# Optimization experiments

Measured on AMD Instinct MI355X. Metric: run time of the kernel, lower is better.

The kernel has to match this reference:

```python
import jax, jax.numpy as jnp
import numpy as np

B, N, C = 4, 2048, 256
H = 8
DH = C // H
WIN = 16
SCALE = DH ** -0.5


def setup_inputs() -> dict:
    key = jax.random.key(0)
    k1, k2, k3, k4 = jax.random.split(key, 4)
    x = jax.random.normal(k1, (B, N, C), dtype=jnp.float32)
    # qkv: nn.Linear(dim, 3*dim, bias=False); store as [C, 3C] for x @ W
    W_qkv = jax.random.normal(k2, (C, 3 * C), dtype=jnp.float32) * (C ** -0.5)
    # proj: nn.Linear(dim, dim) with bias
    W_proj = jax.random.normal(k3, (C, C), dtype=jnp.float32) * (C ** -0.5)
    b_proj = jax.random.normal(k4, (C,), dtype=jnp.float32) * 0.01
    return {"x": x, "W_qkv": W_qkv, "W_proj": W_proj, "b_proj": b_proj}


def reference(x, W_qkv, W_proj, b_proj):
    Bs, Ns, Cs = x.shape
    # qkv projection -> q, k, v each [B, H, N, Dh]
    qkv = (x @ W_qkv).reshape(Bs, Ns, 3, H, DH).transpose(2, 0, 3, 1, 4)
    q, k, v = qkv[0], qkv[1], qkv[2]

    # --- global dense attention ---
    attn_global = jax.nn.softmax(jnp.einsum('bhnd,bhmd->bhnm', q, k) * SCALE, axis=-1)
    x_global = jnp.einsum('bhnm,bhmd->bhnd', attn_global, v)  # [B,H,N,Dh]

    # --- non-overlapping local window attention (vectorized over windows) ---
    nw = Ns // WIN
    qw = q.reshape(Bs, H, nw, WIN, DH)
    kw = k.reshape(Bs, H, nw, WIN, DH)
    vw = v.reshape(Bs, H, nw, WIN, DH)
    attn_local = jax.nn.softmax(jnp.einsum('bhwid,bhwjd->bhwij', qw, kw) * SCALE, axis=-1)
    x_local = jnp.einsum('bhwij,bhwjd->bhwid', attn_local, vw).reshape(Bs, H, Ns, DH)

    # combine, merge heads, output projection
    x_out = (x_global + x_local).transpose(0, 2, 1, 3).reshape(Bs, Ns, Cs)
    x_out = x_out @ W_proj + b_proj
    weights = jax.lax.stop_gradient(attn_global)
    return (x_out, weights)
```

## Files before the change

kernel.cpp:

```cpp
#include <hip/hip_runtime.h>
#include <hip/hip_bf16.h>

#define B_ 4
#define N_ 2048
#define C_ 256
#define H_ 8
#define DH_ 32
#define SCALE_ 0.17677669529663687f

typedef __attribute__((ext_vector_type(8))) short bf16x8;
typedef __attribute__((ext_vector_type(4))) float f32x4;

__device__ __forceinline__ short f2bf(float f) {
    union { float f; unsigned u; } v; v.f = f;
    unsigned r = v.u + 0x7fffu + ((v.u >> 16) & 1u);
    return (short)(r >> 16);
}
__device__ __forceinline__ float bf2f(short s) {
    union { unsigned u; float f; } v; v.u = ((unsigned)(unsigned short)s) << 16;
    return v.f;
}
__device__ __forceinline__ bf16x8 cvt_pk8(f32x4 a, f32x4 b) {
    union { unsigned u[4]; bf16x8 v; } r;
    asm("v_cvt_pk_bf16_f32 %0, %1, %2" : "=v"(r.u[0]) : "v"(a[0]), "v"(a[1]));
    asm("v_cvt_pk_bf16_f32 %0, %1, %2" : "=v"(r.u[1]) : "v"(a[2]), "v"(a[3]));
    asm("v_cvt_pk_bf16_f32 %0, %1, %2" : "=v"(r.u[2]) : "v"(b[0]), "v"(b[1]));
    asm("v_cvt_pk_bf16_f32 %0, %1, %2" : "=v"(r.u[3]) : "v"(b[2]), "v"(b[3]));
    return r.v;
}

__global__ __launch_bounds__(256) void k_qkv(
    const float* __restrict__ x, const float* __restrict__ Wq,
    short* __restrict__ qbf, short* __restrict__ kbf, short* __restrict__ vtbf)
{
    __shared__ __align__(16) short XSh[64*40], XSl[64*40];
    __shared__ __align__(16) short WTh[128*40], WTl[128*40];
    const int tid = threadIdx.x;
    const int wid = tid >> 6, lane = tid & 63;
    const int l15 = lane & 15, quad = lane >> 4;
    const int r0 = blockIdx.y * 64;
    const int c0 = blockIdx.x * 128;

    f32x4 acc[8];
    #pragma unroll
    for (int t = 0; t < 8; ++t) acc[t] = (f32x4){0.f,0.f,0.f,0.f};

    for (int kk = 0; kk < 8; ++kk) {
        const int k0 = kk * 32;
        {
            int row = tid >> 2, cg = tid & 3;
            const float* xp = &x[(size_t)(r0 + row) * C_ + k0 + cg * 8];
            float4 a = *(const float4*)xp;
            float4 b = *(const float4*)(xp + 4);
            float vals[8] = {a.x,a.y,a.z,a.w,b.x,b.y,b.z,b.w};
            short hi[8], lo[8];
            #pragma unroll
            for (int i = 0; i < 8; ++i) {
                hi[i] = f2bf(vals[i]);
                lo[i] = f2bf(vals[i] - bf2f(hi[i]));
            }
            *(bf16x8*)&XSh[row*40 + cg*8] = *(bf16x8*)hi;
            *(bf16x8*)&XSl[row*40 + cg*8] = *(bf16x8*)lo;
        }
        {
            int wrow = tid >> 3, seg = tid & 7;
            const float* wp = &Wq[(size_t)(k0 + wrow) * (3*C_) + c0 + seg*16];
            #pragma unroll
            for (int q4 = 0; q4 < 4; ++q4) {
                float4 wv = *(const float4*)(wp + q4*4);
                float wa[4] = {wv.x, wv.y, wv.z, wv.w};
                #pragma unroll
                for (int i = 0; i < 4; ++i) {
                    int col = seg*16 + q4*4 + i;
                    short hb = f2bf(wa[i]);
                    WTh[col*40 + wrow] = hb;
                    WTl[col*40 + wrow] = f2bf(wa[i] - bf2f(hb));
                }
            }
        }
        __syncthreads();
        bf16x8 ah = *(bf16x8*)&XSh[(wid*16 + l15)*40 + quad*8];
        bf16x8 al = *(bf16x8*)&XSl[(wid*16 + l15)*40 + quad*8];
        #pragma unroll
        for (int t = 0; t < 8; ++t) {
            bf16x8 bh = *(bf16x8*)&WTh[(t*16 + l15)*40 + quad*8];
            bf16x8 bl = *(bf16x8*)&WTl[(t*16 + l15)*40 + quad*8];
            acc[t] = __builtin_amdgcn_mfma_f32_16x16x32_bf16(ah, bh, acc[t], 0,0,0);
            acc[t] = __builtin_amdgcn_mfma_f32_16x16x32_bf16(ah, bl, acc[t], 0,0,0);
            acc[t] = __builtin_amdgcn_mfma_f32_16x16x32_bf16(al, bh, acc[t], 0,0,0);
        }
        __syncthreads();
    }
    #pragma unroll
    for (int t = 0; t < 8; ++t) {
        int j = c0 + t*16 + l15;
        int which = j >> 8, h = (j >> 5) & 7, d = j & 31;
        #pragma unroll
        for (int r = 0; r < 4; ++r) {
            int tok = r0 + wid*16 + quad*4 + r;
            int b = tok >> 11, n = tok & (N_-1);
            float val = acc[t][r];
            int bh = b * H_ + h;
            if (which == 0)      qbf[((size_t)bh * N_ + n) * DH_ + d] = f2bf(val * SCALE_);
            else if (which == 1) kbf[((size_t)bh * N_ + n) * DH_ + d] = f2bf(val);
            else                 vtbf[((size_t)bh * DH_ + d) * N_ + n] = f2bf(val);
        }
    }
}

__global__ __launch_bounds__(256) void k_zsum(
    const short* __restrict__ qbf, const short* __restrict__ kbf,
    float* __restrict__ zrecip)
{
    const int tid = threadIdx.x;
    const int wid = tid >> 6, lane = tid & 63;
    const int l15 = lane & 15, quad = lane >> 4;
    const int bh = blockIdx.y;
    const int q0 = blockIdx.x * 64 + wid * 16;

    bf16x8 aq = *(const bf16x8*)&qbf[((size_t)bh * N_ + q0 + l15) * DH_ + quad * 8];
    float zs[4] = {0.f, 0.f, 0.f, 0.f};
    const short* kbase = &kbf[(size_t)bh * N_ * DH_];
    #pragma unroll 4
    for (int mt = 0; mt < N_/16; ++mt) {
        bf16x8 bk = *(const bf16x8*)&kbase[(mt*16 + l15) * DH_ + quad * 8];
        f32x4 S = __builtin_amdgcn_mfma_f32_16x16x32_bf16(aq, bk, (f32x4){0,0,0,0}, 0,0,0);
        zs[0] += __expf(S[0]); zs[1] += __expf(S[1]);
        zs[2] += __expf(S[2]); zs[3] += __expf(S[3]);
    }
    #pragma unroll
    for (int r = 0; r < 4; ++r)
        for (int off = 1; off < 16; off <<= 1)
            zs[r] += __shfl_xor(zs[r], off, 64);
    if (l15 == 0) {
        #pragma unroll
        for (int r = 0; r < 4; ++r)
            zrecip[(size_t)bh * N_ + q0 + quad*4 + r] = 1.0f / zs[r];
    }
}

__global__ __launch_bounds__(256) void k_attn(
    const short* __restrict__ qbf, const short* __restrict__ kbf,
    const short* __restrict__ vtbf, const float* __restrict__ zrecip,
    float* __restrict__ wout, short* __restrict__ xc)
{
    __shared__ __align__(16) float pt[4][16*36];
    const int tid = threadIdx.x;
    const int wid = tid >> 6, lane = tid & 63;
    const int l15 = lane & 15, quad = lane >> 4;
    const int bh = blockIdx.y;
    const int b = bh >> 3, h = bh & 7;
    const int q0 = blockIdx.x * 64 + wid * 16;
    const int w = q0 >> 4;
    const int mtd = w >> 1, hl = w & 1;

    bf16x8 aq = *(const bf16x8*)&qbf[((size_t)bh * N_ + q0 + l15) * DH_ + quad * 8];
    float zr[4];
    #pragma unroll
    for (int r = 0; r < 4; ++r) zr[r] = zrecip[(size_t)bh * N_ + q0 + quad*4 + r];

    const short* kbase = &kbf[(size_t)bh * N_ * DH_];
    const short* vbase = &vtbf[(size_t)bh * DH_ * N_];
    float* wbase = &wout[((size_t)bh * N_ + q0) * N_];

    f32x4 O0 = {0,0,0,0}, O1 = {0,0,0,0};
    float pl[4] = {0.f,0.f,0.f,0.f};
    float* myp = pt[wid];
    float*       wr0  = &myp[(quad*4)*36 + l15];
    const float* rd   = &myp[l15*36 + quad*8];
    float*       wrow = wbase + (size_t)l15 * N_ + quad*8;

    for (int mt = 0; mt < N_/32; ++mt) {
        const int m0 = mt * 32;
        bf16x8 bk0 = *(const bf16x8*)&kbase[(size_t)(m0 + l15) * DH_ + quad * 8];
        bf16x8 bk1 = *(const bf16x8*)&kbase[(size_t)(m0 + 16 + l15) * DH_ + quad * 8];
        f32x4 S0 = __builtin_amdgcn_mfma_f32_16x16x32_bf16(aq, bk0, (f32x4){0,0,0,0}, 0,0,0);
        f32x4 S1 = __builtin_amdgcn_mfma_f32_16x16x32_bf16(aq, bk1, (f32x4){0,0,0,0}, 0,0,0);
        float p0[4], p1[4];
        #pragma unroll
        for (int r = 0; r < 4; ++r) { p0[r] = __expf(S0[r]); p1[r] = __expf(S1[r]); }
        if (mt == mtd) {
            #pragma unroll
            for (int r = 0; r < 4; ++r) pl[r] = hl ? p1[r] : p0[r];
        }
        #pragma unroll
        for (int r = 0; r < 4; ++r) {
            wr0[r*36]      = p0[r] * zr[r];
            wr0[r*36 + 16] = p1[r] * zr[r];
        }
        f32x4 pa0 = *(const f32x4*)rd;
        f32x4 pa1 = *(const f32x4*)(rd + 4);
        __builtin_nontemporal_store(pa0, (f32x4*)(wrow + m0));
        __builtin_nontemporal_store(pa1, (f32x4*)(wrow + m0 + 4));
        bf16x8 ap = cvt_pk8(pa0, pa1);
        bf16x8 bv0 = *(const bf16x8*)&vbase[(size_t)l15 * N_ + m0 + quad*8];
        bf16x8 bv1 = *(const bf16x8*)&vbase[(size_t)(16 + l15) * N_ + m0 + quad*8];
        O0 = __builtin_amdgcn_mfma_f32_16x16x32_bf16(ap, bv0, O0, 0,0,0);
        O1 = __builtin_amdgcn_mfma_f32_16x16x32_bf16(ap, bv1, O1, 0,0,0);
    }

    float zl[4];
    #pragma unroll
    for (int r = 0; r < 4; ++r) {
        zl[r] = pl[r];
        for (int off = 1; off < 16; off <<= 1)
            zl[r] += __shfl_xor(zl[r], off, 64);
    }
    #pragma unroll
    for (int r = 0; r < 4; ++r) {
        float pn = pl[r] / zl[r];
        wr0[r*36]      = hl ? 0.f : pn;
        wr0[r*36 + 16] = hl ? pn : 0.f;
    }
    {
        const int m0 = mtd * 32;
        f32x4 pa0 = *(const f32x4*)rd;
        f32x4 pa1 = *(const f32x4*)(rd + 4);
        bf16x8 ap = cvt_pk8(pa0, pa1);
        bf16x8 bv0 = *(const bf16x8*)&vbase[(size_t)l15 * N_ + m0 + quad*8];
        bf16x8 bv1 = *(const bf16x8*)&vbase[(size_t)(16 + l15) * N_ + m0 + quad*8];
        O0 = __builtin_amdgcn_mfma_f32_16x16x32_bf16(ap, bv0, O0, 0,0,0);
        O1 = __builtin_amdgcn_mfma_f32_16x16x32_bf16(ap, bv1, O1, 0,0,0);
    }
    #pragma unroll
    for (int r = 0; r < 4; ++r) {
        int n = q0 + quad*4 + r;
        short* xrow = &xc[((size_t)(b * N_ + n)) * C_ + h * DH_];
        xrow[l15]      = f2bf(O0[r]);
        xrow[16 + l15] = f2bf(O1[r]);
    }
}

__global__ __launch_bounds__(256) void k_proj(
    const short* __restrict__ xc, const float* __restrict__ Wp,
    const float* __restrict__ bp, float* __restrict__ out)
{
    __shared__ __align__(16) short WT[64 * 264];
    const int tid = threadIdx.x;
    const int wid = tid >> 6, lane = tid & 63;
    const int l15 = lane & 15, quad = lane >> 4;
    const int c0 = blockIdx.x * 64;
    const int r0 = blockIdx.y * 64;

    {
        int k = tid;
        const float* wp = &Wp[(size_t)k * C_ + c0];
        #pragma unroll
        for (int s = 0; s < 16; ++s) {
            float4 wv = *(const float4*)(wp + s*4);
            float wa[4] = {wv.x, wv.y, wv.z, wv.w};
            #pragma unroll
            for (int i = 0; i < 4; ++i)
                WT[(s*4 + i) * 264 + k] = f2bf(wa[i]);
        }
    }
    __syncthreads();

    f32x4 acc[4];
    #pragma unroll
    for (int t = 0; t < 4; ++t) acc[t] = (f32x4){0,0,0,0};
    const short* xrow = &xc[(size_t)(r0 + wid*16 + l15) * C_];
    #pragma unroll
    for (int kk = 0; kk < 8; ++kk) {
        bf16x8 a = *(const bf16x8*)&xrow[kk*32 + quad*8];
        #pragma unroll
        for (int t = 0; t < 4; ++t) {
            bf16x8 bw = *(bf16x8*)&WT[(t*16 + l15) * 264 + kk*32 + quad*8];
            acc[t] = __builtin_amdgcn_mfma_f32_16x16x32_bf16(a, bw, acc[t], 0,0,0);
        }
    }
    #pragma unroll
    for (int t = 0; t < 4; ++t) {
        int j = c0 + t*16 + l15;
        float bias = bp[j];
        #pragma unroll
        for (int r = 0; r < 4; ++r) {
            int row = r0 + wid*16 + quad*4 + r;
            out[(size_t)row * C_ + j] = acc[t][r] + bias;
        }
    }
}

extern "C" void kernel_launch(void* const* d_in, const int* in_sizes, int n_in,
                              void* d_out, int out_size, void* d_ws, size_t ws_size,
                              hipStream_t stream)
{
    const float* x  = (const float*)d_in[0];
    const float* Wq = (const float*)d_in[1];
    const float* Wp = (const float*)d_in[2];
    const float* bp = (const float*)d_in[3];
    float* out  = (float*)d_out;
    float* wout = out + (size_t)B_ * N_ * C_;

    char* ws = (char*)d_ws;
    short* qbf  = (short*)ws;
    short* kbf  = qbf  + (size_t)B_*H_*N_*DH_;
    short* vtbf = kbf  + (size_t)B_*H_*N_*DH_;
    float* zrecip = (float*)(vtbf + (size_t)B_*H_*N_*DH_);
    short* xc   = (short*)(zrecip + (size_t)B_*H_*N_);

    k_qkv <<<dim3(6, 128),  256, 0, stream>>>(x, Wq, qbf, kbf, vtbf);
    k_zsum<<<dim3(32, 32),  256, 0, stream>>>(qbf, kbf, zrecip);
    k_attn<<<dim3(32, 32),  256, 0, stream>>>(qbf, kbf, vtbf, zrecip, wout, xc);
    k_proj<<<dim3(4, 128),  256, 0, stream>>>(xc, Wp, bp, out);
}
```

Measured before the change: 732.0 us.

## Fuse softmax normalizer pass into attention kernel, swizzle QKV weight LDS

Removes the separate k_zsum kernel and its zrecip buffer. Each attention wave now computes its own row sums of exp(QK^T) in a first pass over K before the main loop. The attention-weight output is now written with direct per-row scalar stores instead of LDS-staged nontemporal float4 stores. The transposed weight tile in the QKV GEMM gets an XOR swizzle to reduce LDS bank conflicts. These changes save a launch and the zrecip traffic, but the narrower, cached stores on the large weights output could raise write cost.

```diff
diff --git a/kernel.cpp b/kernel.cpp
--- a/kernel.cpp
+++ b/kernel.cpp
@@ -64,6 +64,8 @@
         }
         {
             int wrow = tid >> 3, seg = tid & 7;
+            const int swz = (seg & 3) << 3;
+            const int wsw = wrow ^ swz;
             const float* wp = &Wq[(size_t)(k0 + wrow) * (3*C_) + c0 + seg*16];
             #pragma unroll
             for (int q4 = 0; q4 < 4; ++q4) {
@@ -73,8 +75,8 @@
                 for (int i = 0; i < 4; ++i) {
                     int col = seg*16 + q4*4 + i;
                     short hb = f2bf(wa[i]);
-                    WTh[col*40 + wrow] = hb;
-                    WTl[col*40 + wrow] = f2bf(wa[i] - bf2f(hb));
+                    WTh[col*40 + wsw] = hb;
+                    WTl[col*40 + wsw] = f2bf(wa[i] - bf2f(hb));
                 }
             }
         }
@@ -83,8 +85,9 @@
         bf16x8 al = *(bf16x8*)&XSl[(wid*16 + l15)*40 + quad*8];
         #pragma unroll
         for (int t = 0; t < 8; ++t) {
-            bf16x8 bh = *(bf16x8*)&WTh[(t*16 + l15)*40 + quad*8];
-            bf16x8 bl = *(bf16x8*)&WTl[(t*16 + l15)*40 + quad*8];
+            const int rb = (quad*8) ^ ((t & 3) << 3);
+            bf16x8 bh = *(bf16x8*)&WTh[(t*16 + l15)*40 + rb];
+            bf16x8 bl = *(bf16x8*)&WTl[(t*16 + l15)*40 + rb];
             acc[t] = __builtin_amdgcn_mfma_f32_16x16x32_bf16(ah, bh, acc[t], 0,0,0);
             acc[t] = __builtin_amdgcn_mfma_f32_16x16x32_bf16(ah, bl, acc[t], 0,0,0);
             acc[t] = __builtin_amdgcn_mfma_f32_16x16x32_bf16(al, bh, acc[t], 0,0,0);
@@ -108,40 +111,9 @@
     }
 }
 
-__global__ __launch_bounds__(256) void k_zsum(
-    const short* __restrict__ qbf, const short* __restrict__ kbf,
-    float* __restrict__ zrecip)
-{
-    const int tid = threadIdx.x;
-    const int wid = tid >> 6, lane = tid & 63;
-    const int l15 = lane & 15, quad = lane >> 4;
-    const int bh = blockIdx.y;
-    const int q0 = blockIdx.x * 64 + wid * 16;
-
-    bf16x8 aq = *(const bf16x8*)&qbf[((size_t)bh * N_ + q0 + l15) * DH_ + quad * 8];
-    float zs[4] = {0.f, 0.f, 0.f, 0.f};
-    const short* kbase = &kbf[(size_t)bh * N_ * DH_];
-    #pragma unroll 4
-    for (int mt = 0; mt < N_/16; ++mt) {
-        bf16x8 bk = *(const bf16x8*)&kbase[(mt*16 + l15) * DH_ + quad * 8];
-        f32x4 S = __builtin_amdgcn_mfma_f32_16x16x32_bf16(aq, bk, (f32x4){0,0,0,0}, 0,0,0);
-        zs[0] += __expf(S[0]); zs[1] += __expf(S[1]);
-        zs[2] += __expf(S[2]); zs[3] += __expf(S[3]);
-    }
-    #pragma unroll
-    for (int r = 0; r < 4; ++r)
-        for (int off = 1; off < 16; off <<= 1)
-            zs[r] += __shfl_xor(zs[r], off, 64);
-    if (l15 == 0) {
-        #pragma unroll
-        for (int r = 0; r < 4; ++r)
-            zrecip[(size_t)bh * N_ + q0 + quad*4 + r] = 1.0f / zs[r];
-    }
-}
-
 __global__ __launch_bounds__(256) void k_attn(
     const short* __restrict__ qbf, const short* __restrict__ kbf,
-    const short* __restrict__ vtbf, const float* __restrict__ zrecip,
+    const short* __restrict__ vtbf,
     float* __restrict__ wout, short* __restrict__ xc)
 {
     __shared__ __align__(16) float pt[4][16*36];
@@ -155,20 +127,34 @@
     const int mtd = w >> 1, hl = w & 1;
 
     bf16x8 aq = *(const bf16x8*)&qbf[((size_t)bh * N_ + q0 + l15) * DH_ + quad * 8];
-    float zr[4];
-    #pragma unroll
-    for (int r = 0; r < 4; ++r) zr[r] = zrecip[(size_t)bh * N_ + q0 + quad*4 + r];
 
     const short* kbase = &kbf[(size_t)bh * N_ * DH_];
     const short* vbase = &vtbf[(size_t)bh * DH_ * N_];
     float* wbase = &wout[((size_t)bh * N_ + q0) * N_];
+
+    float zs[4] = {0.f, 0.f, 0.f, 0.f};
+    for (int mt = 0; mt < N_/32; ++mt) {
+        const int m0 = mt * 32;
+        bf16x8 bk0 = *(const bf16x8*)&kbase[(size_t)(m0 + l15) * DH_ + quad * 8];
+        bf16x8 bk1 = *(const bf16x8*)&kbase[(size_t)(m0 + 16 + l15) * DH_ + quad * 8];
+        f32x4 S0 = __builtin_amdgcn_mfma_f32_16x16x32_bf16(aq, bk0, (f32x4){0,0,0,0}, 0,0,0);
+        f32x4 S1 = __builtin_amdgcn_mfma_f32_16x16x32_bf16(aq, bk1, (f32x4){0,0,0,0}, 0,0,0);
+        #pragma unroll
+        for (int r = 0; r < 4; ++r) { zs[r] += __expf(S0[r]); zs[r] += __expf(S1[r]); }
+    }
+    float zr[4];
+    #pragma unroll
+    for (int r = 0; r < 4; ++r) {
+        for (int off = 1; off < 16; off <<= 1)
+            zs[r] += __shfl_xor(zs[r], off, 64);
+        zr[r] = 1.0f / zs[r];
+    }
 
     f32x4 O0 = {0,0,0,0}, O1 = {0,0,0,0};
     float pl[4] = {0.f,0.f,0.f,0.f};
     float* myp = pt[wid];
     float*       wr0  = &myp[(quad*4)*36 + l15];
     const float* rd   = &myp[l15*36 + quad*8];
-    float*       wrow = wbase + (size_t)l15 * N_ + quad*8;
 
     for (int mt = 0; mt < N_/32; ++mt) {
         const int m0 = mt * 32;
@@ -185,13 +171,16 @@
         }
         #pragma unroll
         for (int r = 0; r < 4; ++r) {
-            wr0[r*36]      = p0[r] * zr[r];
-            wr0[r*36 + 16] = p1[r] * zr[r];
+            float wp0 = p0[r] * zr[r];
+            float wp1 = p1[r] * zr[r];
+            float* wrow = wbase + (size_t)(quad*4 + r) * N_ + m0;
+            wrow[l15]      = wp0;
+            wrow[16 + l15] = wp1;
+            wr0[r*36]      = wp0;
+            wr0[r*36 + 16] = wp1;
         }
         f32x4 pa0 = *(const f32x4*)rd;
         f32x4 pa1 = *(const f32x4*)(rd + 4);
-        __builtin_nontemporal_store(pa0, (f32x4*)(wrow + m0));
-        __builtin_nontemporal_store(pa1, (f32x4*)(wrow + m0 + 4));
         bf16x8 ap = cvt_pk8(pa0, pa1);
         bf16x8 bv0 = *(const bf16x8*)&vbase[(size_t)l15 * N_ + m0 + quad*8];
         bf16x8 bv1 = *(const bf16x8*)&vbase[(size_t)(16 + l15) * N_ + m0 + quad*8];
@@ -296,11 +285,9 @@
     short* qbf  = (short*)ws;
     short* kbf  = qbf  + (size_t)B_*H_*N_*DH_;
     short* vtbf = kbf  + (size_t)B_*H_*N_*DH_;
-    float* zrecip = (float*)(vtbf + (size_t)B_*H_*N_*DH_);
-    short* xc   = (short*)(zrecip + (size_t)B_*H_*N_);
+    short* xc   = vtbf + (size_t)B_*H_*N_*DH_;
 
     k_qkv <<<dim3(6, 128),  256, 0, stream>>>(x, Wq, qbf, kbf, vtbf);
-    k_zsum<<<dim3(32, 32),  256, 0, stream>>>(qbf, kbf, zrecip);
-    k_attn<<<dim3(32, 32),  256, 0, stream>>>(qbf, kbf, vtbf, zrecip, wout, xc);
+    k_attn<<<dim3(32, 32),  256, 0, stream>>>(qbf, kbf, vtbf, wout, xc);
     k_proj<<<dim3(4, 128),  256, 0, stream>>>(xc, Wp, bp, out);
 }
```

New measurement: 686.4 us. 1.07x faster.
